# Optimization experiments

Measured on AMD Instinct MI355X. Metric: run time of the kernel, lower is better.

## Reference

```python
import jax, jax.numpy as jnp
import numpy as np

N, E, IN_DIM, H_DIM, T = 100000, 3200000, 128, 128, 5000


def gcn_conv(x, W, b, src, dst):
    """PyG GCNConv: symmetric norm with self-loops, linear transform, scatter-add."""
    n = x.shape[0]
    h = x @ W  # [N, h]
    # degree with self-loops (all edge weights = 1)
    deg = jax.ops.segment_sum(jnp.ones(src.shape[0], x.dtype), dst, num_segments=n) + 1.0
    dinv = jax.lax.rsqrt(deg)  # deg >= 1 due to self-loops
    norm = dinv[src] * dinv[dst]  # [E]
    out = jax.ops.segment_sum(h[src] * norm[:, None], dst, num_segments=n)
    out = out + h * (dinv * dinv)[:, None]  # self-loop contribution
    return out + b


def setup_inputs() -> dict:
    key = jax.random.key(0)
    ks = jax.random.split(key, 24)
    s_in = 1.0 / np.sqrt(IN_DIM)
    s_h = 1.0 / np.sqrt(H_DIM)
    return {
        "x": jax.random.normal(ks[0], (N, IN_DIM), jnp.float32),
        "edge_index": jax.random.randint(ks[1], (2, E), 0, N),
        "fake_x": jax.random.normal(ks[2], (N, IN_DIM), jnp.float32),
        "fake_edge_index": jax.random.randint(ks[3], (2, E), 0, N),
        "treat_idx": jax.random.randint(ks[4], (T,), 0, N),
        "control_idx": jax.random.randint(ks[5], (T,), 0, N),
        # GCN layer params
        "W1": jax.random.normal(ks[6], (IN_DIM, H_DIM), jnp.float32) * s_in,
        "b1": jnp.zeros((H_DIM,), jnp.float32),
        "W2": jax.random.normal(ks[7], (H_DIM, H_DIM), jnp.float32) * s_h,
        "b2": jnp.zeros((H_DIM,), jnp.float32),
        # heads
        "Wy1": jax.random.normal(ks[8], (H_DIM, 1), jnp.float32) * s_h,
        "by1": jnp.zeros((1,), jnp.float32),
        "Wy0": jax.random.normal(ks[9], (H_DIM, 1), jnp.float32) * s_h,
        "by0": jnp.zeros((1,), jnp.float32),
        "Wb": jax.random.normal(ks[10], (H_DIM, 2), jnp.float32) * s_h,
        "bb": jnp.zeros((2,), jnp.float32),
        "Wp1": jax.random.normal(ks[11], (H_DIM, H_DIM), jnp.float32) * s_h,
        "bp1": jnp.zeros((H_DIM,), jnp.float32),
        "Wp2": jax.random.normal(ks[12], (H_DIM, 2), jnp.float32) * s_h,
        "bp2": jnp.zeros((2,), jnp.float32),
    }


@jax.custom_vjp
def grl(x):
    return x

def _grl_fwd(x):
    return x, None

def _grl_bwd(_, g):
    return (-g,)

grl.defvjp(_grl_fwd, _grl_bwd)


def reference(x, edge_index, fake_x, fake_edge_index, treat_idx, control_idx,
              W1, b1, W2, b2, Wy1, by1, Wy0, by0, Wb, bb, Wp1, bp1, Wp2, bp2):
    lrelu = jax.nn.leaky_relu  # slope 0.01 matches torch default
    src, dst = edge_index[0], edge_index[1]
    fsrc, fdst = fake_edge_index[0], fake_edge_index[1]

    # layer 1 + relu (dropout is identity in eval mode)
    xZ1 = jax.nn.relu(gcn_conv(x, W1, b1, src, dst))
    xfZ1 = jax.nn.relu(gcn_conv(fake_x, W1, b1, fsrc, fdst))
    # layer 2
    xZ2 = gcn_conv(xZ1, W2, b2, src, dst)
    xfZ2 = gcn_conv(xfZ1, W2, b2, fsrc, fdst)

    y1 = lrelu(xZ2[treat_idx] @ Wy1 + by1).squeeze(-1)
    yc0 = lrelu(xfZ2[treat_idx] @ Wy0 + by0).squeeze(-1)
    y0 = lrelu(xZ2[control_idx] @ Wy0 + by0).squeeze(-1)
    yc1 = lrelu(xfZ2[control_idx] @ Wy1 + by1).squeeze(-1)

    fprob = grl(xZ2) @ Wb + bb
    fprob_f = grl(xfZ2) @ Wb + bb

    tprob = lrelu(lrelu(xZ2 @ Wp1 + bp1) @ Wp2 + bp2)
    tprob_f = lrelu(lrelu(xfZ2 @ Wp1 + bp1) @ Wp2 + bp2)

    return (y1, yc0, y0, yc1, fprob, fprob_f, tprob, tprob_f)
```

## Files before the change

### kernel.cpp

```cpp
#include <hip/hip_runtime.h>

#define DIM 128
#define EPB 8192
#define BINSH 8
#define BINN 256

typedef unsigned int uint32;
typedef __attribute__((ext_vector_type(8))) short short8;
typedef __attribute__((ext_vector_type(4))) float f32x4;

__device__ __forceinline__ uint32 bf16_rtne(float f) {
  uint32 u = __float_as_uint(f);
  return (u + 0x7FFFu + ((u >> 16) & 1u)) >> 16;
}
__device__ __forceinline__ float bf16_to_f(uint32 h) { return __uint_as_float(h << 16); }
__device__ __forceinline__ void unpack2(uint32 u, float& x, float& y) {
  x = __uint_as_float(u << 16);
  y = __uint_as_float(u & 0xFFFF0000u);
}


__launch_bounds__(256)
__global__ void csr_sort_kernel(const int* __restrict__ src, const int* __restrict__ dst,
                                int E, int nb1, uint32* __restrict__ tmp,
                                int* __restrict__ dir) {
  __shared__ uint32 sorted[EPB];
  __shared__ int lcnt[512];
  __shared__ int lbase[512];
  __shared__ int ps[256];
  int t = threadIdx.x;
  int base = blockIdx.x * EPB;

  lcnt[t] = 0;
  lcnt[t + 256] = 0;
  __syncthreads();

  uint32 val[32];
  uint32 br[32];
#pragma unroll
  for (int i = 0; i < 32; ++i) {
    int e = base + i * 256 + t;
    if (e < E) {
      int d = __builtin_nontemporal_load(dst + e);
      int s = __builtin_nontemporal_load(src + e);
      int bin = d >> BINSH;
      val[i] = ((uint32)s << BINSH) | (uint32)(d & (BINN - 1));
      int rank = atomicAdd(&lcnt[bin], 1);
      br[i] = ((uint32)bin << 13) | (uint32)rank;
    } else {
      br[i] = 0xFFFFFFFFu;
    }
  }
  __syncthreads();

  {
    int a0 = lcnt[2 * t], a1 = lcnt[2 * t + 1];
    int psum = a0 + a1;
    ps[t] = psum;
    __syncthreads();
    for (int off = 1; off < 256; off <<= 1) {
      int x = (t >= off) ? ps[t - off] : 0;
      __syncthreads();
      ps[t] += x;
      __syncthreads();
    }
    int ebase = ps[t] - psum;
    lbase[2 * t] = ebase;
    lbase[2 * t + 1] = ebase + a0;
  }
  __syncthreads();

#pragma unroll
  for (int i = 0; i < 32; ++i) {
    if (br[i] != 0xFFFFFFFFu) {
      int bin = br[i] >> 13;
      int rank = br[i] & 0x1FFF;
      sorted[lbase[bin] + rank] = val[i];
    }
  }
  __syncthreads();

  int cnt = min(EPB, E - base);
#pragma unroll
  for (int i = 0; i < 32; ++i) {
    int idx = i * 256 + t;
    if (idx < cnt) tmp[base + idx] = sorted[idx];
  }
  for (int b = t; b <= nb1; b += 256) {
    dir[blockIdx.x * (nb1 + 1) + b] = lbase[b];
  }
}


__launch_bounds__(256)
__global__ void csr_build_kernel(const uint32* __restrict__ tmp, const int* __restrict__ dir,
                                 int nA, int nb1, int N, int binCap,
                                 int* __restrict__ row_beg, int* __restrict__ row_end,
                                 int* __restrict__ cols, float* __restrict__ dinv) {
  __shared__ int rbeg[512];
  __shared__ int rend[512];
  __shared__ int deg[BINN];
  __shared__ int cur[BINN];
  __shared__ int ps[256];
  int j = blockIdx.x;
  int t = threadIdx.x;
  int node0 = j << BINSH;
  int colsBase = j * binCap;

  if (t < BINN) deg[t] = 0;
  for (int i = t; i < nA; i += 256) {
    rbeg[i] = dir[i * (nb1 + 1) + j];
    rend[i] = dir[i * (nb1 + 1) + j + 1];
  }
  __syncthreads();

  for (int i = t; i < nA; i += 256) {
    int b = rbeg[i], en = rend[i];
    for (int q = b; q < en; ++q) {
      atomicAdd(&deg[tmp[(size_t)i * EPB + q] & (BINN - 1)], 1);
    }
  }
  __syncthreads();

  int dv = deg[t];
  ps[t] = dv;
  __syncthreads();
  for (int off = 1; off < 256; off <<= 1) {
    int x = (t >= off) ? ps[t - off] : 0;
    __syncthreads();
    ps[t] += x;
    __syncthreads();
  }
  int ebase = ps[t] - dv;
  cur[t] = ebase;
  int node = node0 + t;
  if (node < N) {
    row_beg[node] = colsBase + ebase;
    row_end[node] = colsBase + ebase + dv;
    dinv[node] = rsqrtf((float)dv + 1.0f);
  }
  __syncthreads();

  for (int i = t; i < nA; i += 256) {
    int b = rbeg[i], en = rend[i];
    for (int q = b; q < en; ++q) {
      uint32 v = tmp[(size_t)i * EPB + q];
      int p = atomicAdd(&cur[v & (BINN - 1)], 1);
      cols[colsBase + p] = (int)(v >> BINSH);
    }
  }
}


__global__ void wsplit_kernel(const float* __restrict__ W, uint4* __restrict__ hi4,
                              uint4* __restrict__ lo4) {
  int tid = blockIdx.x * blockDim.x + threadIdx.x;
  int lane = tid & 63;
  int ks = (tid >> 6) & 3;
  int ct = tid >> 8;
  int col = ct * 16 + (lane & 15);
  int k0 = ks * 32 + ((lane >> 4) << 3);
  uint32 h[8], l[8];
#pragma unroll
  for (int j = 0; j < 8; ++j) {
    float w = W[(size_t)(k0 + j) * DIM + col];
    uint32 hh = bf16_rtne(w);
    float rem = w - bf16_to_f(hh);
    l[j] = bf16_rtne(rem);
    h[j] = hh;
  }
  uint4 H, L;
  H.x = h[0] | (h[1] << 16); H.y = h[2] | (h[3] << 16);
  H.z = h[4] | (h[5] << 16); H.w = h[6] | (h[7] << 16);
  L.x = l[0] | (l[1] << 16); L.y = l[2] | (l[3] << 16);
  L.z = l[4] | (l[5] << 16); L.w = l[6] | (l[7] << 16);
  hi4[tid] = H;
  lo4[tid] = L;
}


__launch_bounds__(256, 3)
__global__ void gemm_mfma_kernel(const float* __restrict__ in, const uint4* __restrict__ wHi,
                                 const uint4* __restrict__ wLo, uint32* __restrict__ outb,
                                 int n, const float* __restrict__ rowscale,
                                 const float* __restrict__ bias, float slope, int in_bf16,
                                 const float* __restrict__ headW,
                                 const float* __restrict__ headB,
                                 float* __restrict__ headOut) {
  __shared__ unsigned short sA[2 * 64 * 128];
  __shared__ unsigned short sO[64 * 128];
  int t = threadIdx.x;
  int row0 = blockIdx.x * 64;

  if (in_bf16) {
    const uint4* in4 = (const uint4*)in;
    int q = t & 15;
    int rl = t >> 4;
#pragma unroll
    for (int i = 0; i < 4; ++i) {
      int row = rl + i * 16;
      int grow = row0 + row;
      uint4 v = make_uint4(0, 0, 0, 0);
      if (grow < n) v = in4[(size_t)grow * 16 + q];
      int sidx = (row * 128 + q * 8) ^ ((row & 7) << 3);
      *(uint4*)&sA[sidx] = v;
    }
  } else {
    int quad = t & 31;
    int r = t >> 5;
#pragma unroll
    for (int i = 0; i < 8; ++i) {
      int row = r + i * 8;
      int grow = row0 + row;
      f32x4 v = (f32x4){0.f, 0.f, 0.f, 0.f};
      if (grow < n) v = *(const f32x4*)(in + (size_t)grow * DIM + quad * 4);
      uint32 h0 = bf16_rtne(v.x), h1 = bf16_rtne(v.y), h2 = bf16_rtne(v.z), h3 = bf16_rtne(v.w);
      uint32 l0 = bf16_rtne(v.x - bf16_to_f(h0));
      uint32 l1 = bf16_rtne(v.y - bf16_to_f(h1));
      uint32 l2 = bf16_rtne(v.z - bf16_to_f(h2));
      uint32 l3 = bf16_rtne(v.w - bf16_to_f(h3));
      int sidx = (row * 128 + quad * 4) ^ ((row & 7) << 3);
      *(uint2*)&sA[sidx] = make_uint2(h0 | (h1 << 16), h2 | (h3 << 16));
      *(uint2*)&sA[64 * 128 + sidx] = make_uint2(l0 | (l1 << 16), l2 | (l3 << 16));
    }
  }
  __syncthreads();

  int lane = t & 63;
  int w = t >> 6;
  int rbase = w * 16;
  f32x4 acc[8];
#pragma unroll
  for (int ct = 0; ct < 8; ++ct) acc[ct] = (f32x4){0.f, 0.f, 0.f, 0.f};

  int fragRow = rbase + (lane & 15);
  int fragSwz = (fragRow & 7) << 3;
#pragma unroll
  for (int ks = 0; ks < 4; ++ks) {
    int cidx = ks * 32 + ((lane >> 4) << 3);
    int sidx = (fragRow * 128 + cidx) ^ fragSwz;
    uint4 au = *(uint4*)&sA[sidx];
    short8 ah = __builtin_bit_cast(short8, au);
    short8 al;
    if (!in_bf16) al = __builtin_bit_cast(short8, *(uint4*)&sA[64 * 128 + sidx]);
#pragma unroll
    for (int ct = 0; ct < 8; ++ct) {
      int widx = (ct * 4 + ks) * 64 + lane;
      short8 bh = __builtin_bit_cast(short8, wHi[widx]);
      short8 bl = __builtin_bit_cast(short8, wLo[widx]);
      if (!in_bf16) acc[ct] = __builtin_amdgcn_mfma_f32_16x16x32_bf16(al, bh, acc[ct], 0, 0, 0);
      acc[ct] = __builtin_amdgcn_mfma_f32_16x16x32_bf16(ah, bl, acc[ct], 0, 0, 0);
      acc[ct] = __builtin_amdgcn_mfma_f32_16x16x32_bf16(ah, bh, acc[ct], 0, 0, 0);
    }
  }

  float rs[4];
#pragma unroll
  for (int r = 0; r < 4; ++r) {
    int grow = row0 + rbase + ((lane >> 4) << 2) + r;
    rs[r] = rowscale ? ((grow < n) ? rowscale[grow] : 0.f) : 1.0f;
  }

  float hp0[4] = {0.f, 0.f, 0.f, 0.f};
  float hp1[4] = {0.f, 0.f, 0.f, 0.f};

#pragma unroll
  for (int ct = 0; ct < 8; ++ct) {
    int col = ct * 16 + (lane & 15);
    float bv = bias ? bias[col] : 0.f;
    float hw0 = 0.f, hw1 = 0.f;
    if (headOut) {
      hw0 = headW[col * 2 + 0];
      hw1 = headW[col * 2 + 1];
    }
#pragma unroll
    for (int r = 0; r < 4; ++r) {
      int rowL = rbase + ((lane >> 4) << 2) + r;
      float v = acc[ct][r] * rs[r] + bv;
      v = (v > 0.f) ? v : v * slope;
      if (outb) {
        int sidx = (rowL * 128 + col) ^ ((rowL & 7) << 3);
        sO[sidx] = (unsigned short)bf16_rtne(v);
      }
      if (headOut) {
        hp0[r] = fmaf(v, hw0, hp0[r]);
        hp1[r] = fmaf(v, hw1, hp1[r]);
      }
    }
  }

  if (headOut) {
    float hb0 = headB[0], hb1 = headB[1];
#pragma unroll
    for (int r = 0; r < 4; ++r) {
      float a = hp0[r], b = hp1[r];
#pragma unroll
      for (int off = 8; off; off >>= 1) {
        a += __shfl_xor(a, off);
        b += __shfl_xor(b, off);
      }
      if ((lane & 15) == 0) {
        int grow = row0 + rbase + ((lane >> 4) << 2) + r;
        if (grow < n) {
          float o0 = a + hb0, o1 = b + hb1;
          headOut[2 * (size_t)grow + 0] = (o0 > 0.f) ? o0 : 0.01f * o0;
          headOut[2 * (size_t)grow + 1] = (o1 > 0.f) ? o1 : 0.01f * o1;
        }
      }
    }
  }

  if (outb) {
    __syncthreads();
#pragma unroll
    for (int it = 0; it < 4; ++it) {
      int s = it * 64 + lane;
      int row = rbase + (s >> 4);
      int sin = s & 15;
      int sidx = row * 128 + ((sin * 8) ^ ((row & 7) << 3));
      uint4 v = *(uint4*)&sO[sidx];
      int grow = row0 + row;
      if (grow < n) *(uint4*)(outb + (size_t)grow * 64 + sin * 4) = v;
    }
  }
}


__launch_bounds__(256)
__global__ void agg_kernel(const uint32* __restrict__ g, const int* __restrict__ row_beg,
                           const int* __restrict__ row_end, const int* __restrict__ cols,
                           const float* __restrict__ dinv, const float* __restrict__ bias,
                           void* __restrict__ out, int n, int relu, int out_bf16,
                           const float* __restrict__ fpW, const float* __restrict__ fpB,
                           float* __restrict__ fpOut) {
  int lane = threadIdx.x & 63;
  int node = (blockIdx.x * blockDim.x + threadIdx.x) >> 6;
  if (node >= n) return;
  int beg = row_beg[node];
  int end = row_end[node];
  float ax, ay;
  unpack2(g[(size_t)node * 64 + lane], ax, ay);
  float bx = 0.f, by = 0.f;
  int e = beg;
  for (; e + 16 <= end; e += 16) {
    int s[16];
#pragma unroll
    for (int i = 0; i < 16; ++i) s[i] = cols[e + i];
    uint32 u[16];
#pragma unroll
    for (int i = 0; i < 16; ++i) u[i] = g[(size_t)s[i] * 64 + lane];
#pragma unroll
    for (int i = 0; i < 16; i += 2) {
      float x0, y0, x1, y1;
      unpack2(u[i], x0, y0);
      unpack2(u[i + 1], x1, y1);
      ax += x0; ay += y0;
      bx += x1; by += y1;
    }
  }
  if (e + 8 <= end) {
    int s[8];
#pragma unroll
    for (int i = 0; i < 8; ++i) s[i] = cols[e + i];
    uint32 u[8];
#pragma unroll
    for (int i = 0; i < 8; ++i) u[i] = g[(size_t)s[i] * 64 + lane];
#pragma unroll
    for (int i = 0; i < 8; i += 2) {
      float x0, y0, x1, y1;
      unpack2(u[i], x0, y0);
      unpack2(u[i + 1], x1, y1);
      ax += x0; ay += y0;
      bx += x1; by += y1;
    }
    e += 8;
  }
  for (; e < end; ++e) {
    uint32 u0 = g[(size_t)cols[e] * 64 + lane];
    float x0, y0;
    unpack2(u0, x0, y0);
    ax += x0;
    ay += y0;
  }
  ax += bx;
  ay += by;
  float di = dinv[node];
  float2 bv = ((const float2*)bias)[lane];
  float ox = fmaf(di, ax, bv.x);
  float oy = fmaf(di, ay, bv.y);
  if (relu) {
    ox = fmaxf(ox, 0.f);
    oy = fmaxf(oy, 0.f);
  }
  if (out_bf16) {
    uint32 pk = bf16_rtne(ox) | (bf16_rtne(oy) << 16);
    ((uint32*)out)[(size_t)node * 64 + lane] = pk;
  } else {
    ((float2*)out)[(size_t)node * 64 + lane] = make_float2(ox, oy);
  }

  if (fpOut) {
    float w00 = fpW[(2 * lane) * 2 + 0];
    float w01 = fpW[(2 * lane) * 2 + 1];
    float w10 = fpW[(2 * lane + 1) * 2 + 0];
    float w11 = fpW[(2 * lane + 1) * 2 + 1];
    float p0 = ox * w00 + oy * w10;
    float p1 = ox * w01 + oy * w11;
#pragma unroll
    for (int off = 32; off; off >>= 1) {
      p0 += __shfl_xor(p0, off);
      p1 += __shfl_xor(p1, off);
    }
    if (lane == 0) {
      fpOut[2 * (size_t)node + 0] = p0 + fpB[0];
      fpOut[2 * (size_t)node + 1] = p1 + fpB[1];
    }
  }
}


__global__ void ydot_kernel(const float* __restrict__ Z, const int* __restrict__ idx,
                            const float* __restrict__ w, const float* __restrict__ b,
                            float* __restrict__ out, int T) {
  int lane = threadIdx.x & 63;
  int t = (blockIdx.x * blockDim.x + threadIdx.x) >> 6;
  if (t >= T) return;
  float2 wv = ((const float2*)w)[lane];
  int node = idx[t];
  float2 z = ((const float2*)Z)[(size_t)node * 64 + lane];
  float pp = z.x * wv.x + z.y * wv.y;
#pragma unroll
  for (int off = 32; off; off >>= 1) pp += __shfl_xor(pp, off);
  if (lane == 0) {
    float o = pp + b[0];
    out[t] = (o > 0.f) ? o : 0.01f * o;
  }
}


extern "C" void kernel_launch(void* const* d_in, const int* in_sizes, int n_in,
                              void* d_out, int out_size, void* d_ws, size_t ws_size,
                              hipStream_t stream) {
  const int N = in_sizes[0] / DIM;
  const int E = in_sizes[1] / 2;
  const int T = in_sizes[4];
  const int nb1 = (N + BINN - 1) >> BINSH;
  const int nA = (E + EPB - 1) / EPB;
  const int binCap = ((E / nb1 + 1024 + 15) / 16) * 16;

  const float* x = (const float*)d_in[0];
  const int* ei = (const int*)d_in[1];
  const float* fx = (const float*)d_in[2];
  const int* fei = (const int*)d_in[3];
  const int* treat = (const int*)d_in[4];
  const int* control = (const int*)d_in[5];
  const float* W1 = (const float*)d_in[6];
  const float* b1 = (const float*)d_in[7];
  const float* W2 = (const float*)d_in[8];
  const float* b2 = (const float*)d_in[9];
  const float* Wy1 = (const float*)d_in[10];
  const float* by1 = (const float*)d_in[11];
  const float* Wy0 = (const float*)d_in[12];
  const float* by0 = (const float*)d_in[13];
  const float* Wb = (const float*)d_in[14];
  const float* bb = (const float*)d_in[15];
  const float* Wp1 = (const float*)d_in[16];
  const float* bp1 = (const float*)d_in[17];
  const float* Wp2 = (const float*)d_in[18];
  const float* bp2 = (const float*)d_in[19];

  float* out = (float*)d_out;

  char* p = (char*)d_ws;
  float* bufZ = (float*)p;   p += (size_t)N * DIM * sizeof(float);
  uint32* bufG = (uint32*)p; p += (size_t)N * (DIM / 2) * sizeof(uint32);
  int* cols = (int*)p;       p += (size_t)nb1 * binCap * sizeof(int);
  int* dir = (int*)p;        p += (size_t)nA * (nb1 + 1) * sizeof(int);
  int* row_beg = (int*)p;    p += (size_t)(N + 16) * sizeof(int);
  int* row_end = (int*)p;    p += (size_t)(N + 16) * sizeof(int);
  float* dinv = (float*)p;   p += (size_t)(N + 16) * sizeof(float);
  uint4* w1Hi = (uint4*)p;   p += 2048 * sizeof(uint4);
  uint4* w1Lo = (uint4*)p;   p += 2048 * sizeof(uint4);
  uint4* w2Hi = (uint4*)p;   p += 2048 * sizeof(uint4);
  uint4* w2Lo = (uint4*)p;   p += 2048 * sizeof(uint4);
  uint4* wp1Hi = (uint4*)p;  p += 2048 * sizeof(uint4);
  uint4* wp1Lo = (uint4*)p;  p += 2048 * sizeof(uint4);
  uint32* tmp = (uint32*)bufZ;

  float* oy1 = out;
  float* oyc0 = out + T;
  float* oy0 = out + 2 * T;
  float* oyc1 = out + 3 * T;
  float* ofp = out + 4 * T;
  float* ofpf = out + 4 * T + 2 * N;
  float* otp = out + 4 * T + 4 * N;
  float* otpf = out + 4 * T + 6 * N;

  wsplit_kernel<<<8, 256, 0, stream>>>(W1, w1Hi, w1Lo);
  wsplit_kernel<<<8, 256, 0, stream>>>(W2, w2Hi, w2Lo);
  wsplit_kernel<<<8, 256, 0, stream>>>(Wp1, wp1Hi, wp1Lo);

  auto run = [&](const float* X, const int* EI,
                 float* y_t, const float* Wt, const float* bt,
                 float* y_c, const float* Wc, const float* bc,
                 float* fp, float* tp) {
    const int* srcp = EI;
    const int* dstp = EI + E;
    csr_sort_kernel<<<nA, 256, 0, stream>>>(srcp, dstp, E, nb1, tmp, dir);
    csr_build_kernel<<<nb1, 256, 0, stream>>>(tmp, dir, nA, nb1, N, binCap,
                                              row_beg, row_end, cols, dinv);
    gemm_mfma_kernel<<<(N + 63) / 64, 256, 0, stream>>>(X, w1Hi, w1Lo, bufG, N, dinv,
                                                        nullptr, 1.0f, 0, nullptr, nullptr, nullptr);
    agg_kernel<<<(N + 3) / 4, 256, 0, stream>>>(bufG, row_beg, row_end, cols, dinv, b1,
                                                (void*)bufZ, N, 1, 1, nullptr, nullptr, nullptr);
    gemm_mfma_kernel<<<(N + 63) / 64, 256, 0, stream>>>(bufZ, w2Hi, w2Lo, bufG, N, dinv,
                                                        nullptr, 1.0f, 1, nullptr, nullptr, nullptr);
    agg_kernel<<<(N + 3) / 4, 256, 0, stream>>>(bufG, row_beg, row_end, cols, dinv, b2,
                                                (void*)bufZ, N, 0, 0, Wb, bb, fp);
    gemm_mfma_kernel<<<(N + 63) / 64, 256, 0, stream>>>(bufZ, wp1Hi, wp1Lo, nullptr, N, nullptr,
                                                        bp1, 0.01f, 0, Wp2, bp2, tp);
    ydot_kernel<<<(T + 3) / 4, 256, 0, stream>>>(bufZ, treat, Wt, bt, y_t, T);
    ydot_kernel<<<(T + 3) / 4, 256, 0, stream>>>(bufZ, control, Wc, bc, y_c, T);
  };

  run(x, ei, oy1, Wy1, by1, oy0, Wy0, by0, ofp, otp);
  run(fx, fei, oyc0, Wy0, by0, oyc1, Wy1, by1, ofpf, otpf);
}
```

Baseline: 875.4 us.

## Stage CSR bin edges in LDS, store layer-2 output as bf16, fuse ydot launches

The CSR build kernel now copies each bin's edges from the scattered sort buffer into shared memory once, using a block-wide scan over the run offsets. It then does the degree count and the column scatter from LDS, so the global buffer is no longer read twice with serial per-thread loops. Bins larger than the staging capacity fall back to the old path. The layer-2 aggregation output is now stored as packed bf16 (a flag flip in the agg and gemm calls), which halves the traffic for the later GEMM and gathers but lowers precision. The two ydot launches are merged into one kernel that reads the bf16 values.

```diff
diff --git a/kernel.cpp b/kernel.cpp
--- a/kernel.cpp
+++ b/kernel.cpp
@@ -4,6 +4,7 @@
 #define EPB 8192
 #define BINSH 8
 #define BINN 256
+#define SORT_CAP 9456
 
 typedef unsigned int uint32;
 typedef __attribute__((ext_vector_type(8))) short short8;
@@ -97,8 +98,10 @@
                                  int nA, int nb1, int N, int binCap,
                                  int* __restrict__ row_beg, int* __restrict__ row_end,
                                  int* __restrict__ cols, float* __restrict__ dinv) {
+  __shared__ uint32 stage[SORT_CAP];
   __shared__ int rbeg[512];
   __shared__ int rend[512];
+  __shared__ int rpos[512];
   __shared__ int deg[BINN];
   __shared__ int cur[BINN];
   __shared__ int ps[256];
@@ -114,39 +117,92 @@
   }
   __syncthreads();
 
-  for (int i = t; i < nA; i += 256) {
-    int b = rbeg[i], en = rend[i];
-    for (int q = b; q < en; ++q) {
-      atomicAdd(&deg[tmp[(size_t)i * EPB + q] & (BINN - 1)], 1);
-    }
-  }
-  __syncthreads();
-
-  int dv = deg[t];
-  ps[t] = dv;
-  __syncthreads();
-  for (int off = 1; off < 256; off <<= 1) {
-    int x = (t >= off) ? ps[t - off] : 0;
-    __syncthreads();
-    ps[t] += x;
-    __syncthreads();
-  }
-  int ebase = ps[t] - dv;
-  cur[t] = ebase;
-  int node = node0 + t;
-  if (node < N) {
-    row_beg[node] = colsBase + ebase;
-    row_end[node] = colsBase + ebase + dv;
-    dinv[node] = rsqrtf((float)dv + 1.0f);
-  }
-  __syncthreads();
-
-  for (int i = t; i < nA; i += 256) {
-    int b = rbeg[i], en = rend[i];
-    for (int q = b; q < en; ++q) {
-      uint32 v = tmp[(size_t)i * EPB + q];
-      int p = atomicAdd(&cur[v & (BINN - 1)], 1);
-      cols[colsBase + p] = (int)(v >> BINSH);
+  {
+    int i0 = 2 * t, i1 = 2 * t + 1;
+    int l0 = (i0 < nA) ? (rend[i0] - rbeg[i0]) : 0;
+    int l1 = (i1 < nA) ? (rend[i1] - rbeg[i1]) : 0;
+    int psum = l0 + l1;
+    ps[t] = psum;
+    __syncthreads();
+    for (int off = 1; off < 256; off <<= 1) {
+      int x = (t >= off) ? ps[t - off] : 0;
+      __syncthreads();
+      ps[t] += x;
+      __syncthreads();
+    }
+    int ebase = ps[t] - psum;
+    if (i0 < nA) rpos[i0] = ebase;
+    if (i1 < nA) rpos[i1] = ebase + l0;
+  }
+  __syncthreads();
+  int cnt = ps[255];
+  __syncthreads();
+
+  if (cnt <= SORT_CAP) {
+    for (int i = 0; i < nA; ++i) {
+      int b = rbeg[i];
+      int len = rend[i] - b;
+      for (int q = t; q < len; q += 256) stage[rpos[i] + q] = tmp[(size_t)i * EPB + b + q];
+    }
+    __syncthreads();
+    for (int p = t; p < cnt; p += 256) atomicAdd(&deg[stage[p] & (BINN - 1)], 1);
+    __syncthreads();
+    int dv = deg[t];
+    ps[t] = dv;
+    __syncthreads();
+    for (int off = 1; off < 256; off <<= 1) {
+      int x = (t >= off) ? ps[t - off] : 0;
+      __syncthreads();
+      ps[t] += x;
+      __syncthreads();
+    }
+    int ebase = ps[t] - dv;
+    cur[t] = ebase;
+    int node = node0 + t;
+    if (node < N) {
+      row_beg[node] = colsBase + ebase;
+      row_end[node] = colsBase + ebase + dv;
+      dinv[node] = rsqrtf((float)dv + 1.0f);
+    }
+    __syncthreads();
+    for (int p = t; p < cnt; p += 256) {
+      uint32 v = stage[p];
+      int q = atomicAdd(&cur[v & (BINN - 1)], 1);
+      cols[colsBase + q] = (int)(v >> BINSH);
+    }
+  } else {
+    for (int i = t; i < nA; i += 256) {
+      int b = rbeg[i], en = rend[i];
+      for (int q = b; q < en; ++q) {
+        atomicAdd(&deg[tmp[(size_t)i * EPB + q] & (BINN - 1)], 1);
+      }
+    }
+    __syncthreads();
+    int dv = deg[t];
+    ps[t] = dv;
+    __syncthreads();
+    for (int off = 1; off < 256; off <<= 1) {
+      int x = (t >= off) ? ps[t - off] : 0;
+      __syncthreads();
+      ps[t] += x;
+      __syncthreads();
+    }
+    int ebase = ps[t] - dv;
+    cur[t] = ebase;
+    int node = node0 + t;
+    if (node < N) {
+      row_beg[node] = colsBase + ebase;
+      row_end[node] = colsBase + ebase + dv;
+      dinv[node] = rsqrtf((float)dv + 1.0f);
+    }
+    __syncthreads();
+    for (int i = t; i < nA; i += 256) {
+      int b = rbeg[i], en = rend[i];
+      for (int q = b; q < en; ++q) {
+        uint32 v = tmp[(size_t)i * EPB + q];
+        int p = atomicAdd(&cur[v & (BINN - 1)], 1);
+        cols[colsBase + p] = (int)(v >> BINSH);
+      }
     }
   }
 }
@@ -419,21 +475,31 @@
 }
 
 
-__global__ void ydot_kernel(const float* __restrict__ Z, const int* __restrict__ idx,
-                            const float* __restrict__ w, const float* __restrict__ b,
-                            float* __restrict__ out, int T) {
+__global__ void ydot2_kernel(const uint32* __restrict__ Z,
+                             const int* __restrict__ idxA, const float* __restrict__ wA,
+                             const float* __restrict__ bA, float* __restrict__ outA,
+                             const int* __restrict__ idxB, const float* __restrict__ wB,
+                             const float* __restrict__ bB, float* __restrict__ outB,
+                             int T) {
   int lane = threadIdx.x & 63;
   int t = (blockIdx.x * blockDim.x + threadIdx.x) >> 6;
-  if (t >= T) return;
+  if (t >= 2 * T) return;
+  int isB = (t >= T);
+  int ti = isB ? (t - T) : t;
+  const int* idx = isB ? idxB : idxA;
+  const float* w = isB ? wB : wA;
+  const float* b = isB ? bB : bA;
+  float* o = isB ? outB : outA;
   float2 wv = ((const float2*)w)[lane];
-  int node = idx[t];
-  float2 z = ((const float2*)Z)[(size_t)node * 64 + lane];
-  float pp = z.x * wv.x + z.y * wv.y;
+  int node = idx[ti];
+  float zx, zy;
+  unpack2(Z[(size_t)node * 64 + lane], zx, zy);
+  float pp = zx * wv.x + zy * wv.y;
 #pragma unroll
   for (int off = 32; off; off >>= 1) pp += __shfl_xor(pp, off);
   if (lane == 0) {
-    float o = pp + b[0];
-    out[t] = (o > 0.f) ? o : 0.01f * o;
+    float v = pp + b[0];
+    o[ti] = (v > 0.f) ? v : 0.01f * v;
   }
 }
 
@@ -516,11 +582,12 @@
     gemm_mfma_kernel<<<(N + 63) / 64, 256, 0, stream>>>(bufZ, w2Hi, w2Lo, bufG, N, dinv,
                                                         nullptr, 1.0f, 1, nullptr, nullptr, nullptr);
     agg_kernel<<<(N + 3) / 4, 256, 0, stream>>>(bufG, row_beg, row_end, cols, dinv, b2,
-                                                (void*)bufZ, N, 0, 0, Wb, bb, fp);
+                                                (void*)bufZ, N, 0, 1, Wb, bb, fp);
     gemm_mfma_kernel<<<(N + 63) / 64, 256, 0, stream>>>(bufZ, wp1Hi, wp1Lo, nullptr, N, nullptr,
-                                                        bp1, 0.01f, 0, Wp2, bp2, tp);
-    ydot_kernel<<<(T + 3) / 4, 256, 0, stream>>>(bufZ, treat, Wt, bt, y_t, T);
-    ydot_kernel<<<(T + 3) / 4, 256, 0, stream>>>(bufZ, control, Wc, bc, y_c, T);
+                                                        bp1, 0.01f, 1, Wp2, bp2, tp);
+    ydot2_kernel<<<(2 * T + 3) / 4, 256, 0, stream>>>((const uint32*)bufZ,
+                                                      treat, Wt, bt, y_t,
+                                                      control, Wc, bc, y_c, T);
   };
 
   run(x, ei, oy1, Wy1, by1, oy0, Wy0, by0, ofp, otp);
```

Measured after the change: 1.076 ms. 23.0% more time.
